# Optimization experiments

Measured on AMD Instinct MI355X. Metric: run time of the kernel, lower is better.

Reference implementation:

```python
import jax, jax.numpy as jnp
import numpy as np

MARGIN = 0.3
EPS = 1e-16


def _pairwise_euclidean(x):
    # torch.cdist(x, x, p=2): sqrt of squared distances via the GEMM trick.
    sq_norms = jnp.sum(x * x, axis=1)  # [N]
    sq = sq_norms[:, None] + sq_norms[None, :] - 2.0 * (x @ x.T)  # [N, N]
    sq = jnp.maximum(sq, 0.0)
    # safe sqrt: zero distance -> zero grad (matches torch.cdist backward)
    pos = sq > 0.0
    return jnp.where(pos, jnp.sqrt(jnp.where(pos, sq, 1.0)), 0.0)


def _triplet_mask(labels):
    n = labels.shape[0]
    eye = jnp.eye(n, dtype=bool)
    not_eq = ~eye
    distinct = not_eq[:, :, None] & not_eq[:, None, :] & not_eq[None, :, :]
    lbl_eq = labels[None, :] == labels[:, None]  # [N, N]
    valid = lbl_eq[:, :, None] & (~lbl_eq[:, None, :])  # i==j label, i!=k label
    return valid & distinct


def setup_inputs() -> dict:
    key = jax.random.key(0)
    k1, k2 = jax.random.split(key)
    embeddings = jax.random.normal(k1, (512, 128), dtype=jnp.float32)
    labels = jax.random.randint(k2, (512,), 0, 50, dtype=jnp.int64 if jax.config.read('jax_enable_x64') else jnp.int32)
    return {"embeddings": embeddings, "labels": labels}


def reference(embeddings, labels):
    d = _pairwise_euclidean(embeddings)  # [N, N]
    # anchor-positive minus anchor-negative, plus margin: [N, N, N]
    triplet = d[:, :, None] - d[:, None, :] + MARGIN
    mask = _triplet_mask(labels)
    triplet = jnp.where(mask, triplet, 0.0)
    triplet = jnp.maximum(triplet, 0.0)  # triplet_loss[triplet_loss < 0] = 0
    num_pos = jnp.sum(triplet > EPS).astype(triplet.dtype)
    return jnp.sum(triplet) / (num_pos + EPS)
```

## Files before the change

kernel.cpp:

```cpp
#include <hip/hip_runtime.h>

#define NN 512
#define DD 128
#define MARGIN_F 0.3f
#define TS 32
#define PADW 132

__global__ __launch_bounds__(256) void dist_tile_kernel(
    const float* __restrict__ x,
    float* __restrict__ D) {

    const int bi = blockIdx.x >> 4;
    const int bj = blockIdx.x & 15;
    const int t  = threadIdx.x;

    __shared__ __align__(16) float As[TS][PADW];
    __shared__ __align__(16) float Bs[TS][PADW];
    __shared__ float nA[TS];
    __shared__ float nB[TS];

    const float4* xa = (const float4*)(x + bi * TS * DD);
    const float4* xb = (const float4*)(x + bj * TS * DD);

#pragma unroll
    for (int it = 0; it < 4; ++it) {
        int f = it * 256 + t;
        int r = f >> 5;
        int c4 = f & 31;
        float4 va = xa[f];
        float4 vb = xb[f];
        *(float4*)&As[r][c4 * 4] = va;
        *(float4*)&Bs[r][c4 * 4] = vb;
        float sa = va.x * va.x + va.y * va.y + va.z * va.z + va.w * va.w;
        float sb = vb.x * vb.x + vb.y * vb.y + vb.z * vb.z + vb.w * vb.w;
#pragma unroll
        for (int m = 16; m >= 1; m >>= 1) {
            sa += __shfl_xor(sa, m, 32);
            sb += __shfl_xor(sb, m, 32);
        }
        if ((t & 31) == 0) { nA[r] = sa; nB[r] = sb; }
    }
    __syncthreads();

    const int ty = t >> 4;
    const int tx = t & 15;
    float acc00 = 0.f, acc01 = 0.f, acc10 = 0.f, acc11 = 0.f;
#pragma unroll
    for (int k4 = 0; k4 < 32; ++k4) {
        float4 a0 = *(const float4*)&As[2 * ty][k4 * 4];
        float4 a1 = *(const float4*)&As[2 * ty + 1][k4 * 4];
        float4 b0 = *(const float4*)&Bs[2 * tx][k4 * 4];
        float4 b1 = *(const float4*)&Bs[2 * tx + 1][k4 * 4];
        acc00 = fmaf(a0.x, b0.x, acc00); acc00 = fmaf(a0.y, b0.y, acc00);
        acc00 = fmaf(a0.z, b0.z, acc00); acc00 = fmaf(a0.w, b0.w, acc00);
        acc01 = fmaf(a0.x, b1.x, acc01); acc01 = fmaf(a0.y, b1.y, acc01);
        acc01 = fmaf(a0.z, b1.z, acc01); acc01 = fmaf(a0.w, b1.w, acc01);
        acc10 = fmaf(a1.x, b0.x, acc10); acc10 = fmaf(a1.y, b0.y, acc10);
        acc10 = fmaf(a1.z, b0.z, acc10); acc10 = fmaf(a1.w, b0.w, acc10);
        acc11 = fmaf(a1.x, b1.x, acc11); acc11 = fmaf(a1.y, b1.y, acc11);
        acc11 = fmaf(a1.z, b1.z, acc11); acc11 = fmaf(a1.w, b1.w, acc11);
    }

    const float n0 = nA[2 * ty], n1 = nA[2 * ty + 1];
    const float m0 = nB[2 * tx], m1 = nB[2 * tx + 1];
    float2 r0, r1;
    r0.x = sqrtf(fmaxf(n0 + m0 - 2.f * acc00, 0.f));
    r0.y = sqrtf(fmaxf(n0 + m1 - 2.f * acc01, 0.f));
    r1.x = sqrtf(fmaxf(n1 + m0 - 2.f * acc10, 0.f));
    r1.y = sqrtf(fmaxf(n1 + m1 - 2.f * acc11, 0.f));
    const int gr = bi * TS + 2 * ty;
    const int gc = bj * TS + 2 * tx;
    *(float2*)&D[gr * NN + gc] = r0;
    *(float2*)&D[(gr + 1) * NN + gc] = r1;
}

__global__ __launch_bounds__(512) void triplet_partial_kernel(
    const float* __restrict__ D,
    const int* __restrict__ labels,
    float* __restrict__ psum,
    unsigned int* __restrict__ pcnt) {

    const int i = blockIdx.x;
    const int tid = threadIdx.x;

    __shared__ int ls[NN];
    __shared__ float tvals[NN];
    __shared__ int npos;
    __shared__ float wsum[8];
    __shared__ unsigned int wcnt[8];

    if (tid == 0) npos = 0;
    const float dj = D[i * NN + tid];
    ls[tid] = labels[tid];
    __syncthreads();

    const int li = ls[i];
    if (ls[tid] == li && tid != i) {
        int p = atomicAdd(&npos, 1);
        tvals[p] = dj + MARGIN_F;
    }
    __syncthreads();

    const int np = npos;
    float lsum = 0.0f;
    unsigned int lcnt = 0u;
    if (ls[tid] != li) {
        for (int p = 0; p < np; ++p) {
            float v = tvals[p] - dj;
            lsum += fmaxf(v, 0.0f);
            lcnt += (v > 1e-16f) ? 1u : 0u;
        }
    }

    for (int off = 32; off > 0; off >>= 1) {
        lsum += __shfl_down(lsum, off);
        lcnt += __shfl_down(lcnt, off);
    }
    const int wave = tid >> 6;
    const int lane = tid & 63;
    if (lane == 0) { wsum[wave] = lsum; wcnt[wave] = lcnt; }
    __syncthreads();

    if (tid == 0) {
        float bs = 0.0f;
        unsigned int bc = 0u;
#pragma unroll
        for (int w = 0; w < 8; ++w) { bs += wsum[w]; bc += wcnt[w]; }
        psum[i] = bs;
        pcnt[i] = bc;
    }
}

__global__ __launch_bounds__(64) void reduce_kernel(
    const float* __restrict__ psum,
    const unsigned int* __restrict__ pcnt,
    float* __restrict__ out) {

    const int tid = threadIdx.x;
    float lsum = 0.0f;
    unsigned int lcnt = 0u;
#pragma unroll
    for (int w = 0; w < NN / 64; ++w) {
        lsum += psum[w * 64 + tid];
        lcnt += pcnt[w * 64 + tid];
    }
    for (int off = 32; off > 0; off >>= 1) {
        lsum += __shfl_down(lsum, off);
        lcnt += __shfl_down(lcnt, off);
    }
    if (tid == 0) out[0] = lsum / ((float)lcnt + 1e-16f);
}

extern "C" void kernel_launch(void* const* d_in, const int* in_sizes, int n_in,
                              void* d_out, int out_size, void* d_ws, size_t ws_size,
                              hipStream_t stream) {
    const float* x = (const float*)d_in[0];
    const int* labels = (const int*)d_in[1];
    float* out = (float*)d_out;

    float* psum = (float*)d_ws;
    unsigned int* pcnt = (unsigned int*)((char*)d_ws + 2048);
    float* Dm = (float*)((char*)d_ws + 4096);

    dist_tile_kernel<<<256, 256, 0, stream>>>(x, Dm);
    triplet_partial_kernel<<<NN, 512, 0, stream>>>(Dm, labels, psum, pcnt);
    reduce_kernel<<<1, 64, 0, stream>>>(psum, pcnt, out);
}
```

Measured before the change: 63.12 us.

## Fuse final reduction into triplet kernel via atomics and swizzle LDS tiles

Removes the separate single-block reduce kernel. Each triplet block now atomically accumulates into 16 slots, and the last block to finish, found with a done counter, reduces the slots and writes the output. The counters are zeroed in the distance kernel. The padded shared-memory tiles are replaced by an XOR-swizzled float4 layout to avoid bank conflicts. This saves one kernel launch in exchange for atomic contention and nondeterministic float summation order.

After: 73.49 us. 1.16x slower.

```diff
diff --git a/kernel.cpp b/kernel.cpp
--- a/kernel.cpp
+++ b/kernel.cpp
@@ -4,18 +4,29 @@
 #define DD 128
 #define MARGIN_F 0.3f
 #define TS 32
-#define PADW 132
+#define NSLOT 16
+
+#define SW(r, c4) ((c4) ^ (((r) >> 1) & 7))
 
 __global__ __launch_bounds__(256) void dist_tile_kernel(
     const float* __restrict__ x,
-    float* __restrict__ D) {
+    float* __restrict__ D,
+    float* __restrict__ gsum,
+    unsigned int* __restrict__ gcnt,
+    unsigned int* __restrict__ ndone) {
 
     const int bi = blockIdx.x >> 4;
     const int bj = blockIdx.x & 15;
     const int t  = threadIdx.x;
 
-    __shared__ __align__(16) float As[TS][PADW];
-    __shared__ __align__(16) float Bs[TS][PADW];
+    if (blockIdx.x == 0) {
+        if (t < NSLOT) gsum[t] = 0.0f;
+        else if (t < 2 * NSLOT) gcnt[t - NSLOT] = 0u;
+        else if (t == 2 * NSLOT) *ndone = 0u;
+    }
+
+    __shared__ float4 As4[TS][32];
+    __shared__ float4 Bs4[TS][32];
     __shared__ float nA[TS];
     __shared__ float nB[TS];
 
@@ -29,8 +40,8 @@
         int c4 = f & 31;
         float4 va = xa[f];
         float4 vb = xb[f];
-        *(float4*)&As[r][c4 * 4] = va;
-        *(float4*)&Bs[r][c4 * 4] = vb;
+        As4[r][SW(r, c4)] = va;
+        Bs4[r][SW(r, c4)] = vb;
         float sa = va.x * va.x + va.y * va.y + va.z * va.z + va.w * va.w;
         float sb = vb.x * vb.x + vb.y * vb.y + vb.z * vb.z + vb.w * vb.w;
 #pragma unroll
@@ -47,10 +58,10 @@
     float acc00 = 0.f, acc01 = 0.f, acc10 = 0.f, acc11 = 0.f;
 #pragma unroll
     for (int k4 = 0; k4 < 32; ++k4) {
-        float4 a0 = *(const float4*)&As[2 * ty][k4 * 4];
-        float4 a1 = *(const float4*)&As[2 * ty + 1][k4 * 4];
-        float4 b0 = *(const float4*)&Bs[2 * tx][k4 * 4];
-        float4 b1 = *(const float4*)&Bs[2 * tx + 1][k4 * 4];
+        float4 a0 = As4[2 * ty][SW(2 * ty, k4)];
+        float4 a1 = As4[2 * ty + 1][SW(2 * ty + 1, k4)];
+        float4 b0 = Bs4[2 * tx][SW(2 * tx, k4)];
+        float4 b1 = Bs4[2 * tx + 1][SW(2 * tx + 1, k4)];
         acc00 = fmaf(a0.x, b0.x, acc00); acc00 = fmaf(a0.y, b0.y, acc00);
         acc00 = fmaf(a0.z, b0.z, acc00); acc00 = fmaf(a0.w, b0.w, acc00);
         acc01 = fmaf(a0.x, b1.x, acc01); acc01 = fmaf(a0.y, b1.y, acc01);
@@ -74,11 +85,13 @@
     *(float2*)&D[(gr + 1) * NN + gc] = r1;
 }
 
-__global__ __launch_bounds__(512) void triplet_partial_kernel(
+__global__ __launch_bounds__(512) void triplet_fused_kernel(
     const float* __restrict__ D,
     const int* __restrict__ labels,
-    float* __restrict__ psum,
-    unsigned int* __restrict__ pcnt) {
+    float* __restrict__ gsum,
+    unsigned int* __restrict__ gcnt,
+    unsigned int* __restrict__ ndone,
+    float* __restrict__ out) {
 
     const int i = blockIdx.x;
     const int tid = threadIdx.x;
@@ -88,6 +101,7 @@
     __shared__ int npos;
     __shared__ float wsum[8];
     __shared__ unsigned int wcnt[8];
+    __shared__ int islast;
 
     if (tid == 0) npos = 0;
     const float dj = D[i * NN + tid];
@@ -126,29 +140,24 @@
         unsigned int bc = 0u;
 #pragma unroll
         for (int w = 0; w < 8; ++w) { bs += wsum[w]; bc += wcnt[w]; }
-        psum[i] = bs;
-        pcnt[i] = bc;
+        atomicAdd(&gsum[i & (NSLOT - 1)], bs);
+        atomicAdd(&gcnt[i & (NSLOT - 1)], bc);
+        __threadfence();
+        unsigned int old = atomicAdd(ndone, 1u);
+        islast = (old == NN - 1) ? 1 : 0;
     }
-}
+    __syncthreads();
 
-__global__ __launch_bounds__(64) void reduce_kernel(
-    const float* __restrict__ psum,
-    const unsigned int* __restrict__ pcnt,
-    float* __restrict__ out) {
-
-    const int tid = threadIdx.x;
-    float lsum = 0.0f;
-    unsigned int lcnt = 0u;
+    if (islast && tid < NSLOT) {
+        float s = atomicAdd(&gsum[tid], 0.0f);
+        unsigned int c = atomicAdd(&gcnt[tid], 0u);
 #pragma unroll
-    for (int w = 0; w < NN / 64; ++w) {
-        lsum += psum[w * 64 + tid];
-        lcnt += pcnt[w * 64 + tid];
+        for (int off = 8; off > 0; off >>= 1) {
+            s += __shfl_down(s, off);
+            c += __shfl_down(c, off);
+        }
+        if (tid == 0) out[0] = s / ((float)c + 1e-16f);
     }
-    for (int off = 32; off > 0; off >>= 1) {
-        lsum += __shfl_down(lsum, off);
-        lcnt += __shfl_down(lcnt, off);
-    }
-    if (tid == 0) out[0] = lsum / ((float)lcnt + 1e-16f);
 }
 
 extern "C" void kernel_launch(void* const* d_in, const int* in_sizes, int n_in,
@@ -158,11 +167,11 @@
     const int* labels = (const int*)d_in[1];
     float* out = (float*)d_out;
 
-    float* psum = (float*)d_ws;
-    unsigned int* pcnt = (unsigned int*)((char*)d_ws + 2048);
+    float* gsum = (float*)d_ws;
+    unsigned int* gcnt = (unsigned int*)((char*)d_ws + 64);
+    unsigned int* ndone = (unsigned int*)((char*)d_ws + 128);
     float* Dm = (float*)((char*)d_ws + 4096);
 
-    dist_tile_kernel<<<256, 256, 0, stream>>>(x, Dm);
-    triplet_partial_kernel<<<NN, 512, 0, stream>>>(Dm, labels, psum, pcnt);
-    reduce_kernel<<<1, 64, 0, stream>>>(psum, pcnt, out);
+    dist_tile_kernel<<<256, 256, 0, stream>>>(x, Dm, gsum, gcnt, ndone);
+    triplet_fused_kernel<<<NN, 512, 0, stream>>>(Dm, labels, gsum, gcnt, ndone, out);
 }
```
